# Kernel tuning notes

Measured on AMD Instinct MI355X. Metric: run time of the kernel, lower is better.

The kernel has to match this reference:

```python
import jax, jax.numpy as jnp
import numpy as np

THETA = 10000.0

def apply_rope(x, positions):
    # x: [B, H, S, D_head], positions: [S] int
    d = x.shape[-1]
    inv_freq = THETA ** (-jnp.arange(0, d, 2, dtype=jnp.float32) / d)  # [d/2]
    ang = positions.astype(jnp.float32)[:, None] * inv_freq[None, :]   # [S, d/2]
    cos, sin = jnp.cos(ang), jnp.sin(ang)                              # broadcast over B,H
    x1, x2 = x[..., 0::2], x[..., 1::2]
    r1 = x1 * cos - x2 * sin
    r2 = x1 * sin + x2 * cos
    return jnp.stack([r1, r2], axis=-1).reshape(x.shape)


def setup_inputs() -> dict:
    key = jax.random.key(0)
    ks = jax.random.split(key, 5)
    B, S, D = 4, 2048, 1024
    scale = 1.0 / np.sqrt(D)
    return {
        "x": jax.random.normal(ks[0], (B, S, D), dtype=jnp.float32),
        "Wq": jax.random.normal(ks[1], (D, D), dtype=jnp.float32) * scale,
        "Wk": jax.random.normal(ks[2], (D, D), dtype=jnp.float32) * scale,
        "Wv": jax.random.normal(ks[3], (D, D), dtype=jnp.float32) * scale,
        "Wo": jax.random.normal(ks[4], (D, D), dtype=jnp.float32) * scale,
        "token_positions": jnp.arange(S, dtype=jnp.int32),
    }


def reference(x, Wq, Wk, Wv, Wo, token_positions):
    B, S, D = x.shape
    H = 16
    hd = D // H
    # fused QKV projection (weights stored [out, in], y = x @ W^T, no bias)
    qkv_w = jnp.concatenate([Wq, Wk, Wv], axis=0)          # [3D, D]
    qkv = x @ qkv_w.T                                      # [B, S, 3D]
    q, k, v = jnp.split(qkv, 3, axis=-1)
    # [B, S, D] -> [B, H, S, hd]
    def split_heads(t):
        return t.reshape(B, S, H, hd).transpose(0, 2, 1, 3)
    q, k, v = split_heads(q), split_heads(k), split_heads(v)
    q = apply_rope(q, token_positions)
    k = apply_rope(k, token_positions)
    scores = jnp.einsum('bhqd,bhkd->bhqk', q, k) / jnp.sqrt(jnp.float32(hd))
    causal = jnp.tril(jnp.ones((S, S), dtype=bool))        # True = attend
    scores = jnp.where(causal[None, None], scores, -jnp.inf)
    attn = jax.nn.softmax(scores, axis=-1)
    out = jnp.einsum('bhqk,bhkd->bhqd', attn, v)           # [B, H, S, hd]
    out = out.transpose(0, 2, 1, 3).reshape(B, S, D)
    return out @ Wo.T
```

## Files before the change

### kernel.cpp

```cpp
#include <hip/hip_runtime.h>
#include <hip/hip_bf16.h>


typedef __bf16 bf16x8 __attribute__((ext_vector_type(8)));
typedef float f32x4 __attribute__((ext_vector_type(4)));
typedef unsigned short u16x8 __attribute__((ext_vector_type(8)));

#define DEV static __device__ __forceinline__

DEV unsigned short f2bf(float f) {
  unsigned int u = __builtin_bit_cast(unsigned int, f);
  u += 0x7FFFu + ((u >> 16) & 1u);
  return (unsigned short)(u >> 16);
}
DEV float bf2f(unsigned short h) {
  unsigned int u = ((unsigned int)h) << 16;
  return __builtin_bit_cast(float, u);
}
DEV bf16x8 ld_bf8(const unsigned short* p) {
  union { u16x8 u; bf16x8 b; } c;
  c.u = *reinterpret_cast<const u16x8*>(p);
  return c.b;
}
DEV unsigned int pk2(float a, float b) {
  unsigned int r;
  asm("v_cvt_pk_bf16_f32 %0, %1, %2" : "=v"(r) : "v"(a), "v"(b));
  return r;
}

DEV void gload_lds16(const unsigned short* src, unsigned short* dst) {
  __builtin_amdgcn_global_load_lds(
      (const __attribute__((address_space(1))) void*)src,
      (__attribute__((address_space(3))) void*)dst, 16, 0, 0);
}

DEV void stage_tile(const unsigned short* g, int ldg, unsigned short* lds,
                    int wave, int lane) {
  int rl = lane >> 3;
  int c16 = lane & 7;
#pragma unroll
  for (int i = 0; i < 4; ++i) {
    int row = i * 32 + wave * 8 + rl;
    int sc16 = c16 ^ (row & 7);
    const unsigned short* src = g + (size_t)row * ldg + sc16 * 8;
    unsigned short* dst = lds + (i * 32 + wave * 8) * 64;
    gload_lds16(src, dst);
  }
}

DEV bf16x8 lds_frag(const unsigned short* lds, int row, int c16) {
  return ld_bf8(lds + row * 64 + ((c16 ^ (row & 7)) << 3));
}

__global__ void k_f32_to_bf16(const float* __restrict__ in,
                              unsigned short* __restrict__ out, int n4) {
  int i = blockIdx.x * blockDim.x + threadIdx.x;
  if (i < n4) {
    float4 v = reinterpret_cast<const float4*>(in)[i];
    uint2 o;
    o.x = pk2(v.x, v.y);
    o.y = pk2(v.z, v.w);
    reinterpret_cast<uint2*>(out)[i] = o;
  }
}

__global__ void k_conv_w(const float* __restrict__ Wq, const float* __restrict__ Wk,
                         const float* __restrict__ Wv, const float* __restrict__ Wo,
                         unsigned short* __restrict__ Wb, unsigned short* __restrict__ Wob) {
  int i = blockIdx.x * blockDim.x + threadIdx.x;
  int which = i >> 18, j = i & 262143;
  const float* src = (which == 0) ? Wq : (which == 1) ? Wk : (which == 2) ? Wv : Wo;
  unsigned short* dst = (which == 3) ? Wob : Wb + (size_t)which * 1048576;
  float4 v = reinterpret_cast<const float4*>(src)[j];
  uint2 o;
  o.x = pk2(v.x, v.y);
  o.y = pk2(v.z, v.w);
  reinterpret_cast<uint2*>(dst)[j] = o;
}

__global__ void k_rope_table(const int* __restrict__ pos, float* __restrict__ tab) {
  int idx = blockIdx.x * blockDim.x + threadIdx.x;
  if (idx >= 2048 * 32) return;
  int s = idx >> 5, i = idx & 31;
  double inv = pow(10000.0, -(double)(2 * i) / 64.0);
  double ang = (double)pos[s] * inv;
  tab[idx * 2]     = (float)cos(ang);
  tab[idx * 2 + 1] = (float)sin(ang);
}

__global__ __launch_bounds__(256) void k_gemm_qkv(
    const unsigned short* __restrict__ A, const unsigned short* __restrict__ W,
    unsigned short* __restrict__ Qh, unsigned short* __restrict__ Kh,
    unsigned short* __restrict__ Vt, const float* __restrict__ tab) {
  const int Kd = 1024, S = 2048;
  __shared__ __align__(16) unsigned short SM[128 * 132];
  unsigned short* As = SM;
  unsigned short* Bs = SM + 8192;
  int id = blockIdx.x;
  int xcd = id & 7, pos = id >> 3;
  int nid = xcd * 192 + pos;
  int nIdx = nid % 24, mIdx = nid / 24;
  int m0 = mIdx * 128, n0 = nIdx * 128;
  int wave = threadIdx.x >> 6, lane = threadIdx.x & 63;
  int wm = wave >> 1, wn = wave & 1;
  int lr = lane & 15, lk = lane >> 4;
  const unsigned short* Ag = A + (size_t)m0 * Kd;
  const unsigned short* Wg = W + (size_t)n0 * Kd;
  f32x4 acc[4][4] = {};
  for (int k0 = 0; k0 < Kd; k0 += 64) {
    stage_tile(Ag + k0, Kd, As, wave, lane);
    stage_tile(Wg + k0, Kd, Bs, wave, lane);
    __syncthreads();
#pragma unroll
    for (int ks = 0; ks < 2; ++ks) {
      bf16x8 a[4], b[4];
#pragma unroll
      for (int fm = 0; fm < 4; ++fm) a[fm] = lds_frag(As, wm * 64 + fm * 16 + lr, ks * 4 + lk);
#pragma unroll
      for (int fn = 0; fn < 4; ++fn) b[fn] = lds_frag(Bs, wn * 64 + fn * 16 + lr, ks * 4 + lk);
#pragma unroll
      for (int fm = 0; fm < 4; ++fm)
#pragma unroll
        for (int fn = 0; fn < 4; ++fn)
          acc[fm][fn] = __builtin_amdgcn_mfma_f32_16x16x32_bf16(a[fm], b[fn], acc[fm][fn], 0, 0, 0);
    }
    __syncthreads();
  }

  int t = nIdx >> 3;
  int b = m0 >> 11, s_base = m0 & 2047;
  if (t == 2) {
#pragma unroll
    for (int fm = 0; fm < 4; ++fm) {
      int r0 = wm * 64 + fm * 16 + lk * 4;
#pragma unroll
      for (int fn = 0; fn < 4; ++fn) {
        int c = wn * 64 + fn * 16 + lr;
        uint2 w;
        w.x = pk2(acc[fm][fn][0], acc[fm][fn][1]);
        w.y = pk2(acc[fm][fn][2], acc[fm][fn][3]);
        *reinterpret_cast<uint2*>(SM + c * 132 + r0) = w;
      }
    }
    __syncthreads();
    int h0 = (nIdx - 16) * 2;
#pragma unroll
    for (int it = 0; it < 16; ++it) {
      int idx2 = it * 256 + threadIdx.x;
      int c = idx2 >> 5, ch = idx2 & 31;
      int h = h0 + (c >> 6), d = c & 63;
      uint2 w = *reinterpret_cast<const uint2*>(SM + c * 132 + ch * 4);
      *reinterpret_cast<uint2*>(Vt + (((size_t)(b * 16 + h) * 64) + d) * S + s_base + ch * 4) = w;
    }
  } else if (t == 1) {
    int h0 = (nIdx & 7) * 2;
#pragma unroll
    for (int fm = 0; fm < 4; ++fm) {
      int r0 = wm * 64 + fm * 16 + lk * 4;
#pragma unroll
      for (int fn = 0; fn < 4; ++fn) {
        int c = wn * 64 + fn * 16 + lr;
        int h = h0 + (c >> 6), d = c & 63;
        int ri = d >> 1;
        bool odd = d & 1;
#pragma unroll
        for (int r = 0; r < 4; ++r) {
          int s = s_base + r0 + r;
          float2 cs = reinterpret_cast<const float2*>(tab)[s * 32 + ri];
          float v = acc[fm][fn][r];
          float other = __shfl_xor(v, 1);
          float res = odd ? (other * cs.y + v * cs.x)
                          : (v * cs.x - other * cs.y);
          Kh[(((size_t)(b * 16 + h)) * S + s) * 64 + d] = f2bf(res);
        }
      }
    }
  } else {
    int h0 = (nIdx & 7) * 2;
#pragma unroll
    for (int fm = 0; fm < 4; ++fm) {
      int r0 = wm * 64 + fm * 16 + lk * 4;
#pragma unroll
      for (int fn = 0; fn < 4; ++fn) {
        int c = wn * 64 + fn * 16 + lr;
        int h = h0 + (c >> 6), d = c & 63;
#pragma unroll
        for (int r = 0; r < 4; ++r) {
          int s = s_base + r0 + r;
          Qh[(((size_t)(b * 16 + h)) * S + s) * 64 + d] = f2bf(acc[fm][fn][r]);
        }
      }
    }
  }
}

__global__ __launch_bounds__(512) void k_attn(
    const unsigned short* __restrict__ Qh, const unsigned short* __restrict__ Kh,
    const unsigned short* __restrict__ Vt, unsigned short* __restrict__ Obuf,
    const float* __restrict__ tab) {
  const int S = 2048;
  const float KF = 0.18033688f;
  const float NEGH = -34.624667f;
  int bh = blockIdx.x;
  int b = bh >> 4, h = bh & 15;
  int wave = threadIdx.x >> 6, lane = threadIdx.x & 63;
  int lr = lane & 15, lk = lane >> 4;
  int yy = (int)gridDim.y - 1 - (int)blockIdx.y;
  int qt = 2 * yy + (wave >> 2);
  int q0 = qt * 128 + (wave & 3) * 32;
  const unsigned short* Qp = Qh + (size_t)bh * S * 64;
  const unsigned short* Kp = Kh + (size_t)bh * S * 64;
  const unsigned short* Vp = Vt + (size_t)bh * 64 * S;

  __shared__ __align__(16) unsigned short Ks[2][64 * 64];
  __shared__ __align__(16) unsigned short Vs[2][64 * 64];
  __shared__ __align__(16) unsigned short P_all[8][32][64];
  char* pw = (char*)&P_all[wave][0][0];

  auto STAGE = [&](int buf, int kv0) {
    int rl = lane >> 3, c16 = lane & 7;
    int row = wave * 8 + rl;
    int sc = (c16 ^ rl) << 3;
    gload_lds16(Kp + (size_t)(kv0 + row) * 64 + sc, &Ks[buf][wave * 8 * 64]);
    gload_lds16(Vp + (size_t)row * S + kv0 + sc,    &Vs[buf][wave * 8 * 64]);
  };

  bf16x8 qb[2][2];
#pragma unroll
  for (int mi = 0; mi < 2; ++mi)
#pragma unroll
    for (int ks = 0; ks < 2; ++ks) {
      int s = q0 + mi * 16 + lr;
      int d0 = ks * 32 + lk * 8;
      uint4 v = *reinterpret_cast<const uint4*>(Qp + (size_t)s * 64 + d0);
      const float4* tp = reinterpret_cast<const float4*>(tab + s * 64 + d0);
      float4 t0 = tp[0], t1 = tp[1];
      float cs[4][2] = {{t0.x, t0.y}, {t0.z, t0.w}, {t1.x, t1.y}, {t1.z, t1.w}};
      unsigned int vv[4] = {v.x, v.y, v.z, v.w};
      union { unsigned int u[4]; bf16x8 bv; } r;
#pragma unroll
      for (int pq = 0; pq < 4; ++pq) {
        float x1 = bf2f((unsigned short)(vv[pq] & 0xFFFF));
        float x2 = bf2f((unsigned short)(vv[pq] >> 16));
        r.u[pq] = pk2(x1 * cs[pq][0] - x2 * cs[pq][1], x1 * cs[pq][1] + x2 * cs[pq][0]);
      }
      qb[mi][ks] = r.bv;
    }

  f32x4 acc_o[4][2] = {};
  float l_run[2] = {0.f, 0.f};
  int my_nt = (q0 + 31) / 64 + 1;
  int NT = 2 * (2 * yy + 1) + 2;

  STAGE(0, 0);
  __syncthreads();

  for (int t = 0; t < NT; ++t) {
    int cur = t & 1;
    if (t + 1 < NT) STAGE(cur ^ 1, (t + 1) * 64);
    if (t < my_nt) {
      int kv0 = t * 64;
      bf16x8 ka[4][2];
#pragma unroll
      for (int ni = 0; ni < 4; ++ni)
#pragma unroll
        for (int ks = 0; ks < 2; ++ks)
          ka[ni][ks] = lds_frag(&Ks[cur][0], ni * 16 + lr, ks * 4 + lk);
      f32x4 st[4][2] = {};
      __builtin_amdgcn_s_setprio(1);
#pragma unroll
      for (int ni = 0; ni < 4; ++ni)
#pragma unroll
        for (int mi = 0; mi < 2; ++mi) {
          st[ni][mi] = __builtin_amdgcn_mfma_f32_16x16x32_bf16(ka[ni][0], qb[mi][0], st[ni][mi], 0, 0, 0);
          st[ni][mi] = __builtin_amdgcn_mfma_f32_16x16x32_bf16(ka[ni][1], qb[mi][1], st[ni][mi], 0, 0, 0);
        }
      __builtin_amdgcn_s_setprio(0);
      bf16x8 va[4][2];
#pragma unroll
      for (int nf = 0; nf < 4; ++nf)
#pragma unroll
        for (int ks = 0; ks < 2; ++ks)
          va[nf][ks] = lds_frag(&Vs[cur][0], nf * 16 + lr, ks * 4 + lk);

      if (kv0 + 63 > q0) {
#pragma unroll
        for (int mi = 0; mi < 2; ++mi) {
          int row = q0 + mi * 16 + lr;
#pragma unroll
          for (int ni = 0; ni < 4; ++ni)
#pragma unroll
            for (int r = 0; r < 4; ++r)
              if (kv0 + ni * 16 + lk * 4 + r > row) st[ni][mi][r] = -3e38f;
        }
      }
#pragma unroll
      for (int mi = 0; mi < 2; ++mi) {
        int prow = mi * 16 + lr;
        char* rowp = pw + prow * 128;
        int swz = (lr & 7) << 4;
        float rs = 0.f;
#pragma unroll
        for (int ni = 0; ni < 4; ++ni) {
          float p0 = __builtin_amdgcn_exp2f(fmaf(st[ni][mi][0], KF, NEGH));
          float p1 = __builtin_amdgcn_exp2f(fmaf(st[ni][mi][1], KF, NEGH));
          float p2 = __builtin_amdgcn_exp2f(fmaf(st[ni][mi][2], KF, NEGH));
          float p3 = __builtin_amdgcn_exp2f(fmaf(st[ni][mi][3], KF, NEGH));
          rs += (p0 + p1) + (p2 + p3);
          uint2 w; w.x = pk2(p0, p1); w.y = pk2(p2, p3);
          *reinterpret_cast<uint2*>(rowp + ((ni * 32 + lk * 8) ^ swz)) = w;
        }
        rs += __shfl_xor(rs, 16);
        rs += __shfl_xor(rs, 32);
        l_run[mi] += rs;
      }
      bf16x8 pb[2][2];
#pragma unroll
      for (int mi = 0; mi < 2; ++mi) {
        int prow = mi * 16 + lr;
        int swz = (lr & 7) << 4;
#pragma unroll
        for (int ks = 0; ks < 2; ++ks)
          pb[mi][ks] = ld_bf8((const unsigned short*)(pw + prow * 128 + ((ks * 64 + lk * 16) ^ swz)));
      }
      __builtin_amdgcn_s_setprio(1);
#pragma unroll
      for (int nf = 0; nf < 4; ++nf)
#pragma unroll
        for (int mi = 0; mi < 2; ++mi) {
          acc_o[nf][mi] = __builtin_amdgcn_mfma_f32_16x16x32_bf16(va[nf][0], pb[mi][0], acc_o[nf][mi], 0, 0, 0);
          acc_o[nf][mi] = __builtin_amdgcn_mfma_f32_16x16x32_bf16(va[nf][1], pb[mi][1], acc_o[nf][mi], 0, 0, 0);
        }
      __builtin_amdgcn_s_setprio(0);
    }
    __syncthreads();
  }

#pragma unroll
  for (int mi = 0; mi < 2; ++mi) {
    float inv_l = 1.f / l_run[mi];
    int q = q0 + mi * 16 + lr;
    size_t base = ((size_t)b * S + q) * 1024 + h * 64;
#pragma unroll
    for (int nf = 0; nf < 4; ++nf) {
      uint2 w;
      w.x = pk2(acc_o[nf][mi][0] * inv_l, acc_o[nf][mi][1] * inv_l);
      w.y = pk2(acc_o[nf][mi][2] * inv_l, acc_o[nf][mi][3] * inv_l);
      *reinterpret_cast<uint2*>(Obuf + base + nf * 16 + lk * 4) = w;
    }
  }
}

__global__ __launch_bounds__(256) void k_gemm_out(
    const unsigned short* __restrict__ A, const unsigned short* __restrict__ W,
    float* __restrict__ C) {
  const int Kd = 1024;
  __shared__ __align__(16) unsigned short As[128 * 64];
  __shared__ __align__(16) unsigned short Bs[128 * 64];
  int id = blockIdx.x;
  int xcd = id & 7, pos = id >> 3;
  int nid = xcd * 64 + pos;
  int nIdx = nid & 7, mIdx = nid >> 3;
  int m0 = mIdx * 128, n0 = nIdx * 128;
  int wave = threadIdx.x >> 6, lane = threadIdx.x & 63;
  int wm = wave >> 1, wn = wave & 1;
  int lr = lane & 15, lk = lane >> 4;
  const unsigned short* Ag = A + (size_t)m0 * Kd;
  const unsigned short* Wg = W + (size_t)n0 * Kd;
  f32x4 acc[4][4] = {};
  for (int k0 = 0; k0 < Kd; k0 += 64) {
    stage_tile(Ag + k0, Kd, As, wave, lane);
    stage_tile(Wg + k0, Kd, Bs, wave, lane);
    __syncthreads();
#pragma unroll
    for (int ks = 0; ks < 2; ++ks) {
      bf16x8 a[4], b[4];
#pragma unroll
      for (int fm = 0; fm < 4; ++fm) a[fm] = lds_frag(As, wm * 64 + fm * 16 + lr, ks * 4 + lk);
#pragma unroll
      for (int fn = 0; fn < 4; ++fn) b[fn] = lds_frag(Bs, wn * 64 + fn * 16 + lr, ks * 4 + lk);
#pragma unroll
      for (int fm = 0; fm < 4; ++fm)
#pragma unroll
        for (int fn = 0; fn < 4; ++fn)
          acc[fm][fn] = __builtin_amdgcn_mfma_f32_16x16x32_bf16(a[fm], b[fn], acc[fm][fn], 0, 0, 0);
    }
    __syncthreads();
  }
#pragma unroll
  for (int fm = 0; fm < 4; ++fm)
#pragma unroll
    for (int fn = 0; fn < 4; ++fn)
#pragma unroll
      for (int r = 0; r < 4; ++r)
        C[(size_t)(m0 + wm * 64 + fm * 16 + lk * 4 + r) * 1024 + n0 + wn * 64 + fn * 16 + lr] =
            acc[fm][fn][r];
}

extern "C" void kernel_launch(void* const* d_in, const int* in_sizes, int n_in,
                              void* d_out, int out_size, void* d_ws, size_t ws_size,
                              hipStream_t stream) {
  const float* x  = (const float*)d_in[0];
  const float* Wq = (const float*)d_in[1];
  const float* Wk = (const float*)d_in[2];
  const float* Wv = (const float*)d_in[3];
  const float* Wo = (const float*)d_in[4];
  const int* pos  = (const int*)d_in[5];
  float* out = (float*)d_out;
  char* ws = (char*)d_ws;

  unsigned short* xb  = (unsigned short*)(ws);
  unsigned short* Wb  = (unsigned short*)(ws + 16777216);
  unsigned short* Wob = (unsigned short*)(ws + 23068672);
  unsigned short* Qh  = (unsigned short*)(ws + 25165824);
  unsigned short* Kh  = (unsigned short*)(ws + 41943040);
  unsigned short* Ob  = (unsigned short*)(ws + 58720256);
  unsigned short* Vt  = (unsigned short*)(ws + 75497472);
  float* tab          = (float*)(ws + 92274688);
  (void)in_sizes; (void)n_in; (void)out_size; (void)ws_size;

  k_f32_to_bf16<<<8192, 256, 0, stream>>>(x, xb, 2097152);
  k_conv_w<<<4096, 256, 0, stream>>>(Wq, Wk, Wv, Wo, Wb, Wob);
  k_rope_table<<<256, 256, 0, stream>>>(pos, tab);

  k_gemm_qkv<<<1536, 256, 0, stream>>>(xb, Wb, Qh, Kh, Vt, tab);
  dim3 ga(64, 8);
  k_attn<<<ga, 512, 0, stream>>>(Qh, Kh, Vt, Ob, tab);
  k_gemm_out<<<512, 256, 0, stream>>>(Ob, Wob, out);
}
```

Before: 169.9 us.

## Merge prep kernels and enlarge QKV GEMM tile to 256x128 with 8 waves

Fuses the three preprocessing kernels (x conversion, weight conversion, RoPE table) into one launch. The QKV GEMM now uses 512-thread blocks computing 256x128 tiles, which halves the block count and raises reuse of the staged weight tile. The V-transpose epilogue now writes straight to global memory instead of bouncing through shared memory, trading coalescing for one less sync and LDS pass. The larger tile adds LDS and register pressure per block and gives fewer blocks to spread across CUs.

```diff
diff --git a/kernel.cpp b/kernel.cpp
--- a/kernel.cpp
+++ b/kernel.cpp
@@ -36,15 +36,32 @@
 
 DEV void stage_tile(const unsigned short* g, int ldg, unsigned short* lds,
                     int wave, int lane) {
-  int rl = lane >> 3;
-  int c16 = lane & 7;
+  int rl = lane >> 3, c16 = lane & 7;
 #pragma unroll
   for (int i = 0; i < 4; ++i) {
     int row = i * 32 + wave * 8 + rl;
     int sc16 = c16 ^ (row & 7);
-    const unsigned short* src = g + (size_t)row * ldg + sc16 * 8;
-    unsigned short* dst = lds + (i * 32 + wave * 8) * 64;
-    gload_lds16(src, dst);
+    gload_lds16(g + (size_t)row * ldg + sc16 * 8, lds + (i * 32 + wave * 8) * 64);
+  }
+}
+DEV void stage_tile8_256(const unsigned short* g, int ldg, unsigned short* lds,
+                         int wave, int lane) {
+  int rl = lane >> 3, c16 = lane & 7;
+#pragma unroll
+  for (int i = 0; i < 4; ++i) {
+    int row = i * 64 + wave * 8 + rl;
+    int sc16 = c16 ^ rl;
+    gload_lds16(g + (size_t)row * ldg + sc16 * 8, lds + (i * 64 + wave * 8) * 64);
+  }
+}
+DEV void stage_tile8_128(const unsigned short* g, int ldg, unsigned short* lds,
+                         int wave, int lane) {
+  int rl = lane >> 3, c16 = lane & 7;
+#pragma unroll
+  for (int i = 0; i < 2; ++i) {
+    int row = i * 64 + wave * 8 + rl;
+    int sc16 = c16 ^ rl;
+    gload_lds16(g + (size_t)row * ldg + sc16 * 8, lds + (i * 64 + wave * 8) * 64);
   }
 }
 
@@ -52,55 +69,48 @@
   return ld_bf8(lds + row * 64 + ((c16 ^ (row & 7)) << 3));
 }
 
-__global__ void k_f32_to_bf16(const float* __restrict__ in,
-                              unsigned short* __restrict__ out, int n4) {
-  int i = blockIdx.x * blockDim.x + threadIdx.x;
-  if (i < n4) {
-    float4 v = reinterpret_cast<const float4*>(in)[i];
-    uint2 o;
-    o.x = pk2(v.x, v.y);
-    o.y = pk2(v.z, v.w);
-    reinterpret_cast<uint2*>(out)[i] = o;
-  }
-}
-
-__global__ void k_conv_w(const float* __restrict__ Wq, const float* __restrict__ Wk,
-                         const float* __restrict__ Wv, const float* __restrict__ Wo,
-                         unsigned short* __restrict__ Wb, unsigned short* __restrict__ Wob) {
-  int i = blockIdx.x * blockDim.x + threadIdx.x;
-  int which = i >> 18, j = i & 262143;
-  const float* src = (which == 0) ? Wq : (which == 1) ? Wk : (which == 2) ? Wv : Wo;
-  unsigned short* dst = (which == 3) ? Wob : Wb + (size_t)which * 1048576;
-  float4 v = reinterpret_cast<const float4*>(src)[j];
-  uint2 o;
-  o.x = pk2(v.x, v.y);
-  o.y = pk2(v.z, v.w);
-  reinterpret_cast<uint2*>(dst)[j] = o;
-}
-
-__global__ void k_rope_table(const int* __restrict__ pos, float* __restrict__ tab) {
-  int idx = blockIdx.x * blockDim.x + threadIdx.x;
-  if (idx >= 2048 * 32) return;
-  int s = idx >> 5, i = idx & 31;
-  double inv = pow(10000.0, -(double)(2 * i) / 64.0);
-  double ang = (double)pos[s] * inv;
-  tab[idx * 2]     = (float)cos(ang);
-  tab[idx * 2 + 1] = (float)sin(ang);
-}
-
-__global__ __launch_bounds__(256) void k_gemm_qkv(
+__global__ __launch_bounds__(256) void k_prep(
+    const float* __restrict__ x, const float* __restrict__ Wq,
+    const float* __restrict__ Wk, const float* __restrict__ Wv,
+    const float* __restrict__ Wo, const int* __restrict__ pos,
+    unsigned short* __restrict__ xb, unsigned short* __restrict__ Wb,
+    unsigned short* __restrict__ Wob, float* __restrict__ tab) {
+  int bid = blockIdx.x;
+  if (bid < 8192) {
+    int i = bid * 256 + threadIdx.x;
+    float4 v = reinterpret_cast<const float4*>(x)[i];
+    uint2 o; o.x = pk2(v.x, v.y); o.y = pk2(v.z, v.w);
+    reinterpret_cast<uint2*>(xb)[i] = o;
+  } else if (bid < 12288) {
+    int i = (bid - 8192) * 256 + threadIdx.x;
+    int which = i >> 18, j = i & 262143;
+    const float* src = (which == 0) ? Wq : (which == 1) ? Wk : (which == 2) ? Wv : Wo;
+    unsigned short* dst = (which == 3) ? Wob : Wb + (size_t)which * 1048576;
+    float4 v = reinterpret_cast<const float4*>(src)[j];
+    uint2 o; o.x = pk2(v.x, v.y); o.y = pk2(v.z, v.w);
+    reinterpret_cast<uint2*>(dst)[j] = o;
+  } else {
+    int idx = (bid - 12288) * 256 + threadIdx.x;
+    int s = idx >> 5, i = idx & 31;
+    double inv = pow(10000.0, -(double)(2 * i) / 64.0);
+    double ang = (double)pos[s] * inv;
+    tab[idx * 2]     = (float)cos(ang);
+    tab[idx * 2 + 1] = (float)sin(ang);
+  }
+}
+
+__global__ __launch_bounds__(512) void k_gemm_qkv(
     const unsigned short* __restrict__ A, const unsigned short* __restrict__ W,
     unsigned short* __restrict__ Qh, unsigned short* __restrict__ Kh,
     unsigned short* __restrict__ Vt, const float* __restrict__ tab) {
   const int Kd = 1024, S = 2048;
-  __shared__ __align__(16) unsigned short SM[128 * 132];
-  unsigned short* As = SM;
-  unsigned short* Bs = SM + 8192;
+  __shared__ __align__(16) unsigned short As[256 * 64];
+  __shared__ __align__(16) unsigned short Bs[128 * 64];
   int id = blockIdx.x;
   int xcd = id & 7, pos = id >> 3;
-  int nid = xcd * 192 + pos;
+  int nid = xcd * 96 + pos;
   int nIdx = nid % 24, mIdx = nid / 24;
-  int m0 = mIdx * 128, n0 = nIdx * 128;
+  int m0 = mIdx * 256, n0 = nIdx * 128;
   int wave = threadIdx.x >> 6, lane = threadIdx.x & 63;
   int wm = wave >> 1, wn = wave & 1;
   int lr = lane & 15, lk = lane >> 4;
@@ -108,8 +118,8 @@
   const unsigned short* Wg = W + (size_t)n0 * Kd;
   f32x4 acc[4][4] = {};
   for (int k0 = 0; k0 < Kd; k0 += 64) {
-    stage_tile(Ag + k0, Kd, As, wave, lane);
-    stage_tile(Wg + k0, Kd, Bs, wave, lane);
+    stage_tile8_256(Ag + k0, Kd, As, wave, lane);
+    stage_tile8_128(Wg + k0, Kd, Bs, wave, lane);
     __syncthreads();
 #pragma unroll
     for (int ks = 0; ks < 2; ++ks) {
@@ -130,27 +140,19 @@
   int t = nIdx >> 3;
   int b = m0 >> 11, s_base = m0 & 2047;
   if (t == 2) {
+    int h0 = (nIdx & 7) * 2;
 #pragma unroll
     for (int fm = 0; fm < 4; ++fm) {
       int r0 = wm * 64 + fm * 16 + lk * 4;
 #pragma unroll
       for (int fn = 0; fn < 4; ++fn) {
         int c = wn * 64 + fn * 16 + lr;
+        int h = h0 + (c >> 6), d = c & 63;
         uint2 w;
         w.x = pk2(acc[fm][fn][0], acc[fm][fn][1]);
         w.y = pk2(acc[fm][fn][2], acc[fm][fn][3]);
-        *reinterpret_cast<uint2*>(SM + c * 132 + r0) = w;
-      }
-    }
-    __syncthreads();
-    int h0 = (nIdx - 16) * 2;
-#pragma unroll
-    for (int it = 0; it < 16; ++it) {
-      int idx2 = it * 256 + threadIdx.x;
-      int c = idx2 >> 5, ch = idx2 & 31;
-      int h = h0 + (c >> 6), d = c & 63;
-      uint2 w = *reinterpret_cast<const uint2*>(SM + c * 132 + ch * 4);
-      *reinterpret_cast<uint2*>(Vt + (((size_t)(b * 16 + h) * 64) + d) * S + s_base + ch * 4) = w;
+        *reinterpret_cast<uint2*>(Vt + (((size_t)(b * 16 + h) * 64) + d) * S + s_base + r0) = w;
+      }
     }
   } else if (t == 1) {
     int h0 = (nIdx & 7) * 2;
@@ -419,11 +421,8 @@
   float* tab          = (float*)(ws + 92274688);
   (void)in_sizes; (void)n_in; (void)out_size; (void)ws_size;
 
-  k_f32_to_bf16<<<8192, 256, 0, stream>>>(x, xb, 2097152);
-  k_conv_w<<<4096, 256, 0, stream>>>(Wq, Wk, Wv, Wo, Wb, Wob);
-  k_rope_table<<<256, 256, 0, stream>>>(pos, tab);
-
-  k_gemm_qkv<<<1536, 256, 0, stream>>>(xb, Wb, Qh, Kh, Vt, tab);
+  k_prep<<<12544, 256, 0, stream>>>(x, Wq, Wk, Wv, Wo, pos, xb, Wb, Wob, tab);
+  k_gemm_qkv<<<768, 512, 0, stream>>>(xb, Wb, Qh, Kh, Vt, tab);
   dim3 ga(64, 8);
   k_attn<<<ga, 512, 0, stream>>>(Qh, Kh, Vt, Ob, tab);
   k_gemm_out<<<512, 256, 0, stream>>>(Ob, Wob, out);
```

Result: slower. 178.2 us (median of 2 runs) (+4.9%).
